# Optimization experiments

Measured on AMD Instinct MI355X. Metric: run time of the kernel, lower is better.

## Reference

```python
import jax, jax.numpy as jnp
import numpy as np

CODE_DIM = 256
HIDDEN = 128
HEADS = 4
N_CODES = 100000
N_SPEC = 256


def setup_inputs() -> dict:
    key = jax.random.key(0)
    ks = jax.random.split(key, 7)
    provider_emb = jax.random.normal(ks[0], (CODE_DIM,), jnp.float32)
    code_embs = jax.random.normal(ks[1], (N_CODES, CODE_DIM), jnp.float32)
    # per-head Linear(code_dim -> hidden): stacked weights [H, D, K] and bias [H, K]
    W = jax.random.normal(ks[2], (HEADS, CODE_DIM, HIDDEN), jnp.float32) / np.sqrt(CODE_DIM)
    b = jax.random.normal(ks[3], (HEADS, HIDDEN), jnp.float32) * 0.01
    # attention vectors a: [H, 2*hidden] (squeezed trailing 1)
    a = jax.random.normal(ks[4], (HEADS, 2 * HIDDEN), jnp.float32) * 0.01
    # classifier Linear(hidden*heads -> num_specialties)
    Wc = jax.random.normal(ks[5], (N_SPEC, HIDDEN * HEADS), jnp.float32) / np.sqrt(HIDDEN * HEADS)
    bc = jax.random.normal(ks[6], (N_SPEC,), jnp.float32) * 0.01
    return {"provider_emb": provider_emb, "code_embs": code_embs,
            "W": W, "b": b, "a": a, "Wc": Wc, "bc": bc}


def reference(provider_emb, code_embs, W, b, a, Wc, bc):
    # provider projection per head: [H, K]
    provider_h = jnp.einsum('d,hdk->hk', provider_emb, W) + b
    # code projection per head: [H, N, K]
    code_h = jnp.einsum('nd,hdk->hnk', code_embs, W) + b[:, None, :]
    a1, a2 = a[:, :HIDDEN], a[:, HIDDEN:]           # split concat attention vec
    # e[h,n] = leaky_relu(provider_h[h].a1[h] + code_h[h,n].a2[h])
    e = jnp.einsum('hk,hk->h', provider_h, a1)[:, None] \
        + jnp.einsum('hnk,hk->hn', code_h, a2)
    e = jnp.where(e >= 0, e, 0.2 * e)               # LeakyReLU(0.2)
    alpha = jax.nn.softmax(e, axis=1)               # softmax over code nodes
    # dropout is identity in eval mode
    agg = jnp.einsum('hn,hnk->hk', alpha, code_h)   # weighted sum per head
    multi_head_output = agg.reshape(-1)             # [H*K]
    specialty_logits = multi_head_output @ Wc.T + bc
    return specialty_logits, multi_head_output
```

## Files before the change

kernel.cpp:

```cpp
#include <hip/hip_runtime.h>
#include <hip/hip_bf16.h>

#define CODE_DIM 256
#define HIDDEN   128
#define HEADS    4
#define N_CODES  100000
#define N_SPEC   256

#define K2_BLOCKS 256
#define K2_TPB    512
#define K2_WPB    (K2_TPB / 64)
#define K2_TOTAL_WAVES (K2_BLOCKS * K2_WPB)

#define WS_V 0
#define WS_C 1024
#define WS_PART 1028
#define PART_STRIDE (HEADS * CODE_DIM + HEADS)

__global__ void k1_prep(const float* __restrict__ pe, const float* __restrict__ W,
                        const float* __restrict__ b, const float* __restrict__ a,
                        float* __restrict__ ws) {
    const int h = blockIdx.x;
    const int d = threadIdx.x;
    __shared__ float a_sh[2 * HIDDEN];
    a_sh[d] = a[h * 2 * HIDDEN + d];
    __syncthreads();

    const float4* wr4 = (const float4*)(W + ((size_t)h * CODE_DIM + d) * HIDDEN);
    float u = 0.f, v = 0.f;
#pragma unroll
    for (int kk = 0; kk < HIDDEN / 4; ++kk) {
        float4 wv = wr4[kk];
        int k = 4 * kk;
        u += wv.x * a_sh[k]            + wv.y * a_sh[k + 1]
           + wv.z * a_sh[k + 2]        + wv.w * a_sh[k + 3];
        v += wv.x * a_sh[HIDDEN + k]     + wv.y * a_sh[HIDDEN + k + 1]
           + wv.z * a_sh[HIDDEN + k + 2] + wv.w * a_sh[HIDDEN + k + 3];
    }
    ws[WS_V + h * CODE_DIM + d] = v;

    float red = pe[d] * u;
    if (d < HIDDEN) red += b[h * HIDDEN + d] * (a_sh[d] + a_sh[HIDDEN + d]);
#pragma unroll
    for (int off = 32; off; off >>= 1) red += __shfl_xor(red, off, 64);
    __shared__ float wsum[4];
    if ((threadIdx.x & 63) == 0) wsum[threadIdx.x >> 6] = red;
    __syncthreads();
    if (threadIdx.x == 0) ws[WS_C + h] = wsum[0] + wsum[1] + wsum[2] + wsum[3];
}

__global__ __launch_bounds__(K2_TPB) void k2_main(const float* __restrict__ code,
                                                  const float* __restrict__ ws_ro,
                                                  float* __restrict__ part) {
    const int lane = threadIdx.x & 63;
    const int w    = threadIdx.x >> 6;
    const int wg   = blockIdx.x * K2_WPB + w;

    float4 vh[HEADS];
    float  ch[HEADS];
#pragma unroll
    for (int h = 0; h < HEADS; ++h) {
        vh[h] = ((const float4*)(ws_ro + WS_V + h * CODE_DIM))[lane];
        ch[h] = ws_ro[WS_C + h];
    }
    float4 acc[HEADS];
    float  dsum[HEADS];
#pragma unroll
    for (int h = 0; h < HEADS; ++h) {
        acc[h] = make_float4(0.f, 0.f, 0.f, 0.f);
        dsum[h] = 0.f;
    }

    const int S = K2_TOTAL_WAVES;
    int n0 = wg;
    float4 x0 = make_float4(0.f, 0.f, 0.f, 0.f);
    float4 x1 = make_float4(0.f, 0.f, 0.f, 0.f);
    if (n0 < N_CODES)     x0 = ((const float4*)(code + (size_t)n0 * CODE_DIM))[lane];
    if (n0 + S < N_CODES) x1 = ((const float4*)(code + (size_t)(n0 + S) * CODE_DIM))[lane];

    for (int n = n0; n < N_CODES; n += S) {
        float4 x2 = make_float4(0.f, 0.f, 0.f, 0.f);
        if (n + 2 * S < N_CODES)
            x2 = ((const float4*)(code + (size_t)(n + 2 * S) * CODE_DIM))[lane];

        float p[HEADS];
#pragma unroll
        for (int h = 0; h < HEADS; ++h)
            p[h] = x0.x * vh[h].x + x0.y * vh[h].y + x0.z * vh[h].z + x0.w * vh[h].w;
#pragma unroll
        for (int off = 32; off; off >>= 1) {
            p[0] += __shfl_xor(p[0], off, 64);
            p[1] += __shfl_xor(p[1], off, 64);
            p[2] += __shfl_xor(p[2], off, 64);
            p[3] += __shfl_xor(p[3], off, 64);
        }
#pragma unroll
        for (int h = 0; h < HEADS; ++h) {
            float e = p[h] + ch[h];
            e = (e >= 0.f) ? e : 0.2f * e;
            float t = __expf(e);
            dsum[h] += t;
            acc[h].x += t * x0.x; acc[h].y += t * x0.y;
            acc[h].z += t * x0.z; acc[h].w += t * x0.w;
        }
        x0 = x1; x1 = x2;
    }

    __shared__ float red[K2_WPB][HEADS * CODE_DIM];
    __shared__ float redd[K2_WPB][HEADS];
#pragma unroll
    for (int h = 0; h < HEADS; ++h)
        ((float4*)(&red[w][h * CODE_DIM]))[lane] = acc[h];
    if (lane == 0) {
#pragma unroll
        for (int h = 0; h < HEADS; ++h) redd[w][h] = dsum[h];
    }
    __syncthreads();

    float* outp = part + (size_t)blockIdx.x * PART_STRIDE;
    for (int o = threadIdx.x; o < HEADS * CODE_DIM; o += K2_TPB) {
        float s = 0.f;
#pragma unroll
        for (int w2 = 0; w2 < K2_WPB; ++w2) s += red[w2][o];
        outp[o] = s;
    }
    if (threadIdx.x < HEADS) {
        float s = 0.f;
#pragma unroll
        for (int w2 = 0; w2 < K2_WPB; ++w2) s += redd[w2][threadIdx.x];
        outp[HEADS * CODE_DIM + threadIdx.x] = s;
    }
}

__global__ void k3_agg(const float* __restrict__ part, const float* __restrict__ W,
                       const float* __restrict__ b, float* __restrict__ out) {
    const int h   = blockIdx.x;
    const int tid = threadIdx.x;

    float sacc = 0.f;
    const float* p = part + h * CODE_DIM + tid;
#pragma unroll 8
    for (int bb = 0; bb < K2_BLOCKS; ++bb) sacc += p[(size_t)bb * PART_STRIDE];

    float dd = part[(size_t)tid * PART_STRIDE + HEADS * CODE_DIM + h];
#pragma unroll
    for (int off = 32; off; off >>= 1) dd += __shfl_xor(dd, off, 64);
    __shared__ float wred[4];
    __shared__ float den_sh;
    if ((tid & 63) == 0) wred[tid >> 6] = dd;
    __syncthreads();
    if (tid == 0) den_sh = wred[0] + wred[1] + wred[2] + wred[3];
    __syncthreads();

    __shared__ float s_sh[CODE_DIM];
    s_sh[tid] = sacc / den_sh;
    __syncthreads();

    const int k    = tid & (HIDDEN - 1);
    const int half = tid >> 7;
    float y = 0.f;
    const float* wp = W + ((size_t)h * CODE_DIM + half * 128) * HIDDEN + k;
#pragma unroll 8
    for (int d = 0; d < 128; ++d) y += s_sh[half * 128 + d] * wp[(size_t)d * HIDDEN];
    __shared__ float ysh[HIDDEN];
    if (half == 1) ysh[k] = y;
    __syncthreads();
    if (half == 0)
        out[N_SPEC + h * HIDDEN + k] = y + ysh[k] + b[h * HIDDEN + k];
}

__global__ void k4_logits(const float* __restrict__ Wc, const float* __restrict__ bc,
                          float* __restrict__ out) {
    const int lane = threadIdx.x & 63;
    const int wv   = threadIdx.x >> 6;
    const int i    = blockIdx.x * 4 + wv;
    const float4* wr  = (const float4*)(Wc + (size_t)i * (HEADS * HIDDEN));
    const float4* mh4 = (const float4*)(out + N_SPEC);
    float4 wa = wr[lane],      ma = mh4[lane];
    float4 wb = wr[64 + lane], mb = mh4[64 + lane];
    float pp = wa.x * ma.x + wa.y * ma.y + wa.z * ma.z + wa.w * ma.w
             + wb.x * mb.x + wb.y * mb.y + wb.z * mb.z + wb.w * mb.w;
#pragma unroll
    for (int off = 32; off; off >>= 1) pp += __shfl_xor(pp, off, 64);
    if (lane == 0) out[i] = pp + bc[i];
}

extern "C" void kernel_launch(void* const* d_in, const int* in_sizes, int n_in,
                              void* d_out, int out_size, void* d_ws, size_t ws_size,
                              hipStream_t stream) {
    const float* pe   = (const float*)d_in[0];
    const float* code = (const float*)d_in[1];
    const float* W    = (const float*)d_in[2];
    const float* b    = (const float*)d_in[3];
    const float* a    = (const float*)d_in[4];
    const float* Wc   = (const float*)d_in[5];
    const float* bc   = (const float*)d_in[6];
    float* out = (float*)d_out;
    float* ws  = (float*)d_ws;

    k1_prep<<<HEADS, 256, 0, stream>>>(pe, W, b, a, ws);
    k2_main<<<K2_BLOCKS, K2_TPB, 0, stream>>>(code, ws, ws + WS_PART);
    k3_agg<<<HEADS, 256, 0, stream>>>(ws + WS_PART, W, b, out);
    k4_logits<<<64, 256, 0, stream>>>(Wc, bc, out);
}
```

Before: 210.4 us.

## Stage code tiles via global_load_lds, atomic slot reduction, wider prep/agg grids

The main kernel now streams 8-row tiles of code embeddings straight into LDS with global_load_lds. It computes the four head scores by splitting each row across 8 lanes, then accumulates the weighted sums from LDS. Partial results go into 64 atomically updated slots instead of per-block partials, with the slots zeroed in the prep kernel. The prep and aggregation kernels each move from 4 blocks to 16. The aim is more parallelism and better bandwidth use on the 100MB stream, at the cost of explicit waitcnt handling, no overlap between load and compute within a wave, and float atomics.

```diff
diff --git a/kernel.cpp b/kernel.cpp
--- a/kernel.cpp
+++ b/kernel.cpp
@@ -7,166 +7,213 @@
 #define N_CODES  100000
 #define N_SPEC   256
 
-#define K2_BLOCKS 256
-#define K2_TPB    512
-#define K2_WPB    (K2_TPB / 64)
-#define K2_TOTAL_WAVES (K2_BLOCKS * K2_WPB)
-
-#define WS_V 0
-#define WS_C 1024
-#define WS_PART 1028
-#define PART_STRIDE (HEADS * CODE_DIM + HEADS)
+#define K2_BLOCKS 1024
+#define K2_TPB    256
+#define K2_WPB    4
+#define K2_WAVES  (K2_BLOCKS * K2_WPB)
+#define WROWS     8
+#define NTILES    (N_CODES / WROWS)
+#define RSTRIDE   260
+#define NSLOTS    64
+
+#define WS_V       0
+#define WS_CP      1024
+#define WS_SLOT    1040
+#define SLOT_STRIDE 1028
+
+#define LDS_VSH   0
+#define LDS_TSH   1024
+#define LDS_TILE  1152
+#define LDS_TOTAL (LDS_TILE + K2_WPB * WROWS * RSTRIDE)
+
+#define WAITCNT_VM0   0x0F70
+#define WAITCNT_LGKM0 0xC07F
+
+typedef __attribute__((address_space(1))) const void* as1cv;
+typedef __attribute__((address_space(3))) void*       as3v;
 
 __global__ void k1_prep(const float* __restrict__ pe, const float* __restrict__ W,
                         const float* __restrict__ b, const float* __restrict__ a,
                         float* __restrict__ ws) {
-    const int h = blockIdx.x;
-    const int d = threadIdx.x;
+    const int bx = blockIdx.x;
+    const int h = bx >> 2, dq = bx & 3;
+    const int tid = threadIdx.x;
+    const int dl = tid >> 2, q = tid & 3;
+    const int d = dq * 64 + dl;
     __shared__ float a_sh[2 * HIDDEN];
-    a_sh[d] = a[h * 2 * HIDDEN + d];
-    __syncthreads();
-
-    const float4* wr4 = (const float4*)(W + ((size_t)h * CODE_DIM + d) * HIDDEN);
+    __shared__ float cred[4];
+    a_sh[tid] = a[h * 2 * HIDDEN + tid];
+    __syncthreads();
+
+    const float4* wr = (const float4*)(W + ((size_t)(h * CODE_DIM + d)) * HIDDEN + q * 32);
     float u = 0.f, v = 0.f;
 #pragma unroll
-    for (int kk = 0; kk < HIDDEN / 4; ++kk) {
-        float4 wv = wr4[kk];
-        int k = 4 * kk;
-        u += wv.x * a_sh[k]            + wv.y * a_sh[k + 1]
-           + wv.z * a_sh[k + 2]        + wv.w * a_sh[k + 3];
+    for (int j = 0; j < 8; ++j) {
+        float4 wv = wr[j];
+        int k = q * 32 + j * 4;
+        u += wv.x * a_sh[k]     + wv.y * a_sh[k + 1]
+           + wv.z * a_sh[k + 2] + wv.w * a_sh[k + 3];
         v += wv.x * a_sh[HIDDEN + k]     + wv.y * a_sh[HIDDEN + k + 1]
            + wv.z * a_sh[HIDDEN + k + 2] + wv.w * a_sh[HIDDEN + k + 3];
     }
-    ws[WS_V + h * CODE_DIM + d] = v;
-
-    float red = pe[d] * u;
-    if (d < HIDDEN) red += b[h * HIDDEN + d] * (a_sh[d] + a_sh[HIDDEN + d]);
-#pragma unroll
-    for (int off = 32; off; off >>= 1) red += __shfl_xor(red, off, 64);
-    __shared__ float wsum[4];
-    if ((threadIdx.x & 63) == 0) wsum[threadIdx.x >> 6] = red;
-    __syncthreads();
-    if (threadIdx.x == 0) ws[WS_C + h] = wsum[0] + wsum[1] + wsum[2] + wsum[3];
-}
-
-__global__ __launch_bounds__(K2_TPB) void k2_main(const float* __restrict__ code,
-                                                  const float* __restrict__ ws_ro,
-                                                  float* __restrict__ part) {
-    const int lane = threadIdx.x & 63;
-    const int w    = threadIdx.x >> 6;
-    const int wg   = blockIdx.x * K2_WPB + w;
-
-    float4 vh[HEADS];
-    float  ch[HEADS];
+    u += __shfl_xor(u, 1, 64); u += __shfl_xor(u, 2, 64);
+    v += __shfl_xor(v, 1, 64); v += __shfl_xor(v, 2, 64);
+    if (q == 0) ws[WS_V + h * CODE_DIM + d] = v;
+
+    float cp = (q == 0) ? pe[d] * u : 0.f;
+    if (dq == 0 && tid < HIDDEN) cp += b[h * HIDDEN + tid] * (a_sh[tid] + a_sh[HIDDEN + tid]);
+#pragma unroll
+    for (int off = 32; off; off >>= 1) cp += __shfl_xor(cp, off, 64);
+    if ((tid & 63) == 0) cred[tid >> 6] = cp;
+    __syncthreads();
+    if (tid == 0) ws[WS_CP + h * 4 + dq] = cred[0] + cred[1] + cred[2] + cred[3];
+
+    float4* z = (float4*)(ws + WS_SLOT);
+    const int g = bx * 256 + tid;
+#pragma unroll
+    for (int i = 0; i < 5; ++i) {
+        int idx = g + i * 4096;
+        if (idx < (NSLOTS * SLOT_STRIDE) / 4) z[idx] = make_float4(0.f, 0.f, 0.f, 0.f);
+    }
+}
+
+__global__ __launch_bounds__(K2_TPB, 4) void k2_main(const float* __restrict__ code,
+                                                     float* __restrict__ ws) {
+    __shared__ float lds[LDS_TOTAL];
+    const int tid  = threadIdx.x;
+    const int lane = tid & 63;
+    const int w    = tid >> 6;
+    const int row  = lane >> 3;
+    const int seg  = lane & 7;
+    const int bx   = blockIdx.x;
+
+    {
+        float4 vv = ((const float4*)(ws + WS_V))[tid];
+        *(float4*)&lds[LDS_VSH + tid * 4] = vv;
+    }
+    float ch[HEADS];
 #pragma unroll
     for (int h = 0; h < HEADS; ++h) {
-        vh[h] = ((const float4*)(ws_ro + WS_V + h * CODE_DIM))[lane];
-        ch[h] = ws_ro[WS_C + h];
-    }
-    float4 acc[HEADS];
-    float  dsum[HEADS];
-#pragma unroll
-    for (int h = 0; h < HEADS; ++h) {
-        acc[h] = make_float4(0.f, 0.f, 0.f, 0.f);
-        dsum[h] = 0.f;
-    }
-
-    const int S = K2_TOTAL_WAVES;
-    int n0 = wg;
-    float4 x0 = make_float4(0.f, 0.f, 0.f, 0.f);
-    float4 x1 = make_float4(0.f, 0.f, 0.f, 0.f);
-    if (n0 < N_CODES)     x0 = ((const float4*)(code + (size_t)n0 * CODE_DIM))[lane];
-    if (n0 + S < N_CODES) x1 = ((const float4*)(code + (size_t)(n0 + S) * CODE_DIM))[lane];
-
-    for (int n = n0; n < N_CODES; n += S) {
-        float4 x2 = make_float4(0.f, 0.f, 0.f, 0.f);
-        if (n + 2 * S < N_CODES)
-            x2 = ((const float4*)(code + (size_t)(n + 2 * S) * CODE_DIM))[lane];
-
-        float p[HEADS];
-#pragma unroll
-        for (int h = 0; h < HEADS; ++h)
-            p[h] = x0.x * vh[h].x + x0.y * vh[h].y + x0.z * vh[h].z + x0.w * vh[h].w;
-#pragma unroll
-        for (int off = 32; off; off >>= 1) {
-            p[0] += __shfl_xor(p[0], off, 64);
-            p[1] += __shfl_xor(p[1], off, 64);
-            p[2] += __shfl_xor(p[2], off, 64);
-            p[3] += __shfl_xor(p[3], off, 64);
-        }
-#pragma unroll
-        for (int h = 0; h < HEADS; ++h) {
-            float e = p[h] + ch[h];
-            e = (e >= 0.f) ? e : 0.2f * e;
-            float t = __expf(e);
-            dsum[h] += t;
-            acc[h].x += t * x0.x; acc[h].y += t * x0.y;
-            acc[h].z += t * x0.z; acc[h].w += t * x0.w;
-        }
-        x0 = x1; x1 = x2;
-    }
-
-    __shared__ float red[K2_WPB][HEADS * CODE_DIM];
-    __shared__ float redd[K2_WPB][HEADS];
-#pragma unroll
-    for (int h = 0; h < HEADS; ++h)
-        ((float4*)(&red[w][h * CODE_DIM]))[lane] = acc[h];
-    if (lane == 0) {
-#pragma unroll
-        for (int h = 0; h < HEADS; ++h) redd[w][h] = dsum[h];
-    }
-    __syncthreads();
-
-    float* outp = part + (size_t)blockIdx.x * PART_STRIDE;
-    for (int o = threadIdx.x; o < HEADS * CODE_DIM; o += K2_TPB) {
-        float s = 0.f;
-#pragma unroll
-        for (int w2 = 0; w2 < K2_WPB; ++w2) s += red[w2][o];
-        outp[o] = s;
-    }
-    if (threadIdx.x < HEADS) {
-        float s = 0.f;
-#pragma unroll
-        for (int w2 = 0; w2 < K2_WPB; ++w2) s += redd[w2][threadIdx.x];
-        outp[HEADS * CODE_DIM + threadIdx.x] = s;
-    }
-}
-
-__global__ void k3_agg(const float* __restrict__ part, const float* __restrict__ W,
-                       const float* __restrict__ b, float* __restrict__ out) {
-    const int h   = blockIdx.x;
+        float4 cc = *(const float4*)(ws + WS_CP + 4 * h);
+        ch[h] = cc.x + cc.y + cc.z + cc.w;
+    }
+    __syncthreads();
+
+    const int tilebase = LDS_TILE + w * (WROWS * RSTRIDE);
+    const int xb = tilebase + row * RSTRIDE + seg * 32;
+
+    float4 acc0 = make_float4(0,0,0,0), acc1 = acc0, acc2 = acc0, acc3 = acc0;
+    float ds0 = 0.f, ds1 = 0.f, ds2 = 0.f, ds3 = 0.f;
+
+    for (int tile = bx * K2_WPB + w; tile < NTILES; tile += K2_WAVES) {
+        __builtin_amdgcn_s_waitcnt(WAITCNT_LGKM0);
+        const float* gbase = code + (size_t)tile * (WROWS * CODE_DIM) + lane * 4;
+#pragma unroll
+        for (int r = 0; r < WROWS; ++r) {
+            __builtin_amdgcn_global_load_lds((as1cv)(gbase + r * CODE_DIM),
+                                             (as3v)&lds[tilebase + r * RSTRIDE], 16, 0, 0);
+        }
+        __builtin_amdgcn_s_waitcnt(WAITCNT_VM0);
+
+        float p0 = 0.f, p1 = 0.f, p2 = 0.f, p3 = 0.f;
+#pragma unroll
+        for (int c = 0; c < 8; ++c) {
+            float4 x4 = *(const float4*)&lds[xb + c * 4];
+            float4 va = *(const float4*)&lds[LDS_VSH +   0 + seg * 32 + c * 4];
+            float4 vb = *(const float4*)&lds[LDS_VSH + 256 + seg * 32 + c * 4];
+            float4 vc = *(const float4*)&lds[LDS_VSH + 512 + seg * 32 + c * 4];
+            float4 vd = *(const float4*)&lds[LDS_VSH + 768 + seg * 32 + c * 4];
+            p0 += x4.x * va.x + x4.y * va.y + x4.z * va.z + x4.w * va.w;
+            p1 += x4.x * vb.x + x4.y * vb.y + x4.z * vb.z + x4.w * vb.w;
+            p2 += x4.x * vc.x + x4.y * vc.y + x4.z * vc.z + x4.w * vc.w;
+            p3 += x4.x * vd.x + x4.y * vd.y + x4.z * vd.z + x4.w * vd.w;
+        }
+#pragma unroll
+        for (int off = 1; off < 8; off <<= 1) {
+            p0 += __shfl_xor(p0, off, 64);
+            p1 += __shfl_xor(p1, off, 64);
+            p2 += __shfl_xor(p2, off, 64);
+            p3 += __shfl_xor(p3, off, 64);
+        }
+        float e0 = p0 + ch[0]; e0 = (e0 >= 0.f) ? e0 : 0.2f * e0; float t0 = __expf(e0);
+        float e1 = p1 + ch[1]; e1 = (e1 >= 0.f) ? e1 : 0.2f * e1; float t1 = __expf(e1);
+        float e2 = p2 + ch[2]; e2 = (e2 >= 0.f) ? e2 : 0.2f * e2; float t2 = __expf(e2);
+        float e3 = p3 + ch[3]; e3 = (e3 >= 0.f) ? e3 : 0.2f * e3; float t3 = __expf(e3);
+        ds0 += t0; ds1 += t1; ds2 += t2; ds3 += t3;
+        if (seg == 0) *(float4*)&lds[LDS_TSH + w * 32 + row * 4] = make_float4(t0, t1, t2, t3);
+        __builtin_amdgcn_s_waitcnt(WAITCNT_LGKM0);
+
+#pragma unroll
+        for (int r = 0; r < WROWS; ++r) {
+            float4 tr = *(const float4*)&lds[LDS_TSH + w * 32 + r * 4];
+            float4 x4 = *(const float4*)&lds[tilebase + r * RSTRIDE + lane * 4];
+            acc0.x += tr.x * x4.x; acc0.y += tr.x * x4.y; acc0.z += tr.x * x4.z; acc0.w += tr.x * x4.w;
+            acc1.x += tr.y * x4.x; acc1.y += tr.y * x4.y; acc1.z += tr.y * x4.z; acc1.w += tr.y * x4.w;
+            acc2.x += tr.z * x4.x; acc2.y += tr.z * x4.y; acc2.z += tr.z * x4.z; acc2.w += tr.z * x4.w;
+            acc3.x += tr.w * x4.x; acc3.y += tr.w * x4.y; acc3.z += tr.w * x4.z; acc3.w += tr.w * x4.w;
+        }
+    }
+
+    __syncthreads();
+    *(float4*)&lds[w * 1024 +   0 + 4 * lane] = acc0;
+    *(float4*)&lds[w * 1024 + 256 + 4 * lane] = acc1;
+    *(float4*)&lds[w * 1024 + 512 + 4 * lane] = acc2;
+    *(float4*)&lds[w * 1024 + 768 + 4 * lane] = acc3;
+    *(float4*)&lds[4096 + (w * 64 + lane) * 4] = make_float4(ds0, ds1, ds2, ds3);
+    __syncthreads();
+
+    float* slot = ws + WS_SLOT + (size_t)(bx & (NSLOTS - 1)) * SLOT_STRIDE;
+    for (int o = tid; o < HEADS * CODE_DIM; o += K2_TPB) {
+        float s = lds[o] + lds[1024 + o] + lds[2048 + o] + lds[3072 + o];
+        atomicAdd(slot + o, s);
+    }
+    {
+        const int h = tid >> 6, l2 = tid & 63;
+        float dv = lds[4096 +   0 + l2 * 4 + h] + lds[4096 + 256 + l2 * 4 + h]
+                 + lds[4096 + 512 + l2 * 4 + h] + lds[4096 + 768 + l2 * 4 + h];
+#pragma unroll
+        for (int off = 32; off; off >>= 1) dv += __shfl_xor(dv, off, 64);
+        if (l2 == 0) atomicAdd(slot + HEADS * CODE_DIM + h, dv * 0.125f);
+    }
+}
+
+__global__ void k3_agg(const float* __restrict__ W, const float* __restrict__ b,
+                       const float* __restrict__ ws, float* __restrict__ out) {
+    const int bx = blockIdx.x;
+    const int h = bx >> 2, q = bx & 3;
     const int tid = threadIdx.x;
-
-    float sacc = 0.f;
-    const float* p = part + h * CODE_DIM + tid;
+    __shared__ float s_sh[CODE_DIM];
+    __shared__ float yred[8 * 32];
+    __shared__ float den_sh;
+    const float* slots = ws + WS_SLOT;
+
+    if (tid < 64) {
+        float dv = slots[(size_t)tid * SLOT_STRIDE + HEADS * CODE_DIM + h];
+#pragma unroll
+        for (int off = 32; off; off >>= 1) dv += __shfl_xor(dv, off, 64);
+        if (tid == 0) den_sh = dv;
+    }
+    float su = 0.f;
 #pragma unroll 8
-    for (int bb = 0; bb < K2_BLOCKS; ++bb) sacc += p[(size_t)bb * PART_STRIDE];
-
-    float dd = part[(size_t)tid * PART_STRIDE + HEADS * CODE_DIM + h];
-#pragma unroll
-    for (int off = 32; off; off >>= 1) dd += __shfl_xor(dd, off, 64);
-    __shared__ float wred[4];
-    __shared__ float den_sh;
-    if ((tid & 63) == 0) wred[tid >> 6] = dd;
-    __syncthreads();
-    if (tid == 0) den_sh = wred[0] + wred[1] + wred[2] + wred[3];
-    __syncthreads();
-
-    __shared__ float s_sh[CODE_DIM];
-    s_sh[tid] = sacc / den_sh;
-    __syncthreads();
-
-    const int k    = tid & (HIDDEN - 1);
-    const int half = tid >> 7;
+    for (int s2 = 0; s2 < NSLOTS; ++s2)
+        su += slots[(size_t)s2 * SLOT_STRIDE + h * CODE_DIM + tid];
+    __syncthreads();
+    s_sh[tid] = su / den_sh;
+    __syncthreads();
+
+    const int c = tid >> 5, kl = tid & 31;
     float y = 0.f;
-    const float* wp = W + ((size_t)h * CODE_DIM + half * 128) * HIDDEN + k;
+    const float* wp = W + ((size_t)(h * CODE_DIM + c * 32)) * HIDDEN + q * 32 + kl;
 #pragma unroll 8
-    for (int d = 0; d < 128; ++d) y += s_sh[half * 128 + d] * wp[(size_t)d * HIDDEN];
-    __shared__ float ysh[HIDDEN];
-    if (half == 1) ysh[k] = y;
-    __syncthreads();
-    if (half == 0)
-        out[N_SPEC + h * HIDDEN + k] = y + ysh[k] + b[h * HIDDEN + k];
+    for (int d = 0; d < 32; ++d) y += s_sh[c * 32 + d] * wp[(size_t)d * HIDDEN];
+    yred[c * 32 + kl] = y;
+    __syncthreads();
+    if (tid < 32) {
+        float t = 0.f;
+#pragma unroll
+        for (int cc = 0; cc < 8; ++cc) t += yred[cc * 32 + tid];
+        out[N_SPEC + h * HIDDEN + q * 32 + tid] = t + b[h * HIDDEN + q * 32 + tid];
+    }
 }
 
 __global__ void k4_logits(const float* __restrict__ Wc, const float* __restrict__ bc,
@@ -198,8 +245,8 @@
     float* out = (float*)d_out;
     float* ws  = (float*)d_ws;
 
-    k1_prep<<<HEADS, 256, 0, stream>>>(pe, W, b, a, ws);
-    k2_main<<<K2_BLOCKS, K2_TPB, 0, stream>>>(code, ws, ws + WS_PART);
-    k3_agg<<<HEADS, 256, 0, stream>>>(ws + WS_PART, W, b, out);
+    k1_prep<<<16, 256, 0, stream>>>(pe, W, b, a, ws);
+    k2_main<<<K2_BLOCKS, K2_TPB, 0, stream>>>(code, ws);
+    k3_agg<<<16, 256, 0, stream>>>(W, b, ws, out);
     k4_logits<<<64, 256, 0, stream>>>(Wc, bc, out);
 }
```

Result: faster. 177.9 us (-15.4%).
